# Kernel optimization log

Measured on AMD Instinct MI355X. Metric: run time of the kernel, lower is better.

## Reference

```python
import jax, jax.numpy as jnp
import numpy as np

W_DIM = 512
C_IN = 512
C_OUT = 512
K = 3
EPS = 1e-6
STYLE_SCALE = 1.0 / np.sqrt(W_DIM)              # EqualizedWeight scale for (out,in)
CONV_SCALE = 1.0 / np.sqrt(C_IN * K * K)        # EqualizedWeight scale for (out,in,k,k)


def setup_inputs() -> dict:
    key = jax.random.key(0)
    ks = jax.random.split(key, 6)
    B, H, W = 16, 64, 64
    return {
        "x": jax.random.normal(ks[0], (B, C_IN, H, W), dtype=jnp.float32),
        "w": jax.random.normal(ks[1], (B, W_DIM), dtype=jnp.float32),
        "style_weight": jax.random.normal(ks[2], (C_IN, W_DIM), dtype=jnp.float32),
        "style_bias": jnp.zeros((C_IN,), dtype=jnp.float32),
        "conv_weight": jax.random.normal(ks[3], (C_OUT, C_IN, K, K), dtype=jnp.float32),
        "noise_weight": jax.random.normal(ks[4], (1, C_OUT, 1, 1), dtype=jnp.float32),
        "bias": jnp.zeros((C_OUT,), dtype=jnp.float32),
        "noise": jax.random.normal(ks[5], (B, 1, H, W), dtype=jnp.float32),
    }


def reference(x, w, style_weight, style_bias, conv_weight, noise_weight, bias, noise):
    B, _, H, Wd = x.shape
    # to_style: equalized linear  [B, C_IN]
    s = w @ (style_weight * STYLE_SCALE).T + style_bias
    # modulate: [B, C_OUT, C_IN, K, K]
    wts = (conv_weight * CONV_SCALE)[None] * s[:, None, :, None, None]
    # demodulate
    sigma = jax.lax.rsqrt(jnp.sum(wts * wts, axis=(2, 3, 4)) + EPS)  # [B, C_OUT]
    wts = wts * sigma[:, :, None, None, None]
    # grouped conv with groups = batch
    x_r = x.reshape(1, B * C_IN, H, Wd)
    w_r = wts.reshape(B * C_OUT, C_IN, K, K)
    y = jax.lax.conv_general_dilated(
        x_r, w_r, window_strides=(1, 1), padding=[(1, 1), (1, 1)],
        dimension_numbers=("NCHW", "OIHW", "NCHW"), feature_group_count=B,
    ).reshape(B, C_OUT, H, Wd)
    # noise injection + bias + leaky relu(0.2)
    y = y + noise_weight * noise + bias[None, :, None, None]
    return jax.nn.leaky_relu(y, negative_slope=0.2)
```

## Files before the change

### kernel.cpp

```cpp
#include <hip/hip_runtime.h>


typedef __attribute__((ext_vector_type(8))) short short8;
typedef __attribute__((ext_vector_type(4))) float f32x4;

#define STYLE_SCALE 0.044194173824159216f
#define CONV_SCALE  0.014731391274719742f
#define CS2         (1.0f/4608.0f)

static __device__ __forceinline__ unsigned short f2bf(float x) {
    union { float f; unsigned int u; } a; a.f = x;
    unsigned int r = a.u + 0x7fffu + ((a.u >> 16) & 1u);
    return (unsigned short)(r >> 16);
}

static __device__ __forceinline__ void gl_lds16(const void* g, void* l) {
    __builtin_amdgcn_global_load_lds(
        (const __attribute__((address_space(1))) unsigned int*)g,
        (__attribute__((address_space(3))) unsigned int*)l, 16, 0, 0);
}

__global__ void k_style(const float* __restrict__ w, const float* __restrict__ sw,
                        const float* __restrict__ sb, float* __restrict__ s) {
    int b = blockIdx.x, t = threadIdx.x;
    __shared__ float wl[512];
    wl[t]       = w[b*512 + t];
    wl[t + 256] = w[b*512 + t + 256];
    __syncthreads();
    for (int j = t; j < 512; j += 256) {
        const float4* row = (const float4*)(sw + j*512);
        float acc = 0.f;
#pragma unroll 4
        for (int k = 0; k < 128; ++k) {
            float4 v = row[k];
            acc += v.x*wl[4*k] + v.y*wl[4*k+1] + v.z*wl[4*k+2] + v.w*wl[4*k+3];
        }
        s[b*512 + j] = acc * STYLE_SCALE + sb[j];
    }
}

__global__ void k_csq(const float* __restrict__ cw, float* __restrict__ csq) {
    int o = blockIdx.x, t = threadIdx.x;
    for (int i = t; i < 512; i += 256) {
        const float* p = cw + (size_t)(o*512 + i)*9;
        float a = 0.f;
#pragma unroll
        for (int k = 0; k < 9; ++k) { float v = p[k]; a += v*v; }
        csq[o*512 + i] = a * CS2;
    }
}

__global__ void k_sigma(const float* __restrict__ s, const float* __restrict__ csq,
                        float* __restrict__ sig) {
    int b = blockIdx.x, t = threadIdx.x;
    __shared__ float s2[512];
    float v0 = s[b*512 + t], v1 = s[b*512 + t + 256];
    s2[t] = v0*v0; s2[t+256] = v1*v1;
    __syncthreads();
    for (int o = t; o < 512; o += 256) {
        const float4* row = (const float4*)(csq + o*512);
        float acc = 0.f;
#pragma unroll 4
        for (int k = 0; k < 128; ++k) {
            float4 c = row[k];
            acc += c.x*s2[4*k] + c.y*s2[4*k+1] + c.z*s2[4*k+2] + c.w*s2[4*k+3];
        }
        sig[b*512 + o] = 1.0f / sqrtf(acc + 1e-6f);
    }
}

__global__ void k_xt(const float* __restrict__ x, const float* __restrict__ s,
                     unsigned short* __restrict__ xt) {
    int h = blockIdx.x, b = blockIdx.y, t = threadIdx.x;
    __shared__ float tile[64][65];
    for (int c0 = 0; c0 < 512; c0 += 64) {
        for (int it = 0; it < 16; ++it) {
            int idx = t + it*256, c = idx >> 6, wq = idx & 63;
            tile[c][wq] = x[((size_t)(b*512 + c0 + c)*64 + h)*64 + wq];
        }
        __syncthreads();
        for (int it = 0; it < 4; ++it) {
            int idx = t + it*256;
            int wq = idx >> 4, c = (idx & 15) * 4;
            float s0 = s[b*512 + c0 + c],     s1 = s[b*512 + c0 + c + 1];
            float s2v = s[b*512 + c0 + c + 2], s3 = s[b*512 + c0 + c + 3];
            ushort4 pk;
            pk.x = f2bf(tile[c][wq]   * s0);
            pk.y = f2bf(tile[c+1][wq] * s1);
            pk.z = f2bf(tile[c+2][wq] * s2v);
            pk.w = f2bf(tile[c+3][wq] * s3);
            *(ushort4*)(xt + ((size_t)(b*4096 + h*64 + wq)*512 + c0 + c)) = pk;
        }
        __syncthreads();
    }
}

__global__ void k_cwt(const float* __restrict__ cw, unsigned short* __restrict__ cwt) {
    int p = blockIdx.x;
    int g = p & 3, pt = p >> 2;
    int tap = pt % 9, ic = pt / 9;
    int i0 = ic*32 + g*8;
    int t = threadIdx.x;
    for (int o = t; o < 512; o += 256) {
        union { unsigned short us[8]; uint4 q; } u;
#pragma unroll
        for (int j = 0; j < 8; ++j)
            u.us[j] = f2bf(cw[((size_t)o*512 + i0 + j)*9 + tap] * CONV_SCALE);
        *(uint4*)(cwt + ((size_t)p*512 + o)*8) = u.q;
    }
}

__global__ __launch_bounds__(256, 2)
void k_conv(const unsigned short* __restrict__ xt, const unsigned short* __restrict__ cwt,
            const float* __restrict__ sig, const float* __restrict__ nw,
            const float* __restrict__ bias, const float* __restrict__ noise,
            float* __restrict__ out) {
    __shared__ short xs_s[6*66*32];
    __shared__ short wsm_s[9*4*64*8];

    const int tid  = threadIdx.x;
    const int lane = tid & 63;
    const int wave = tid >> 6;
    const int quad = lane >> 4;
    const int l15  = lane & 15;

    const int b     = blockIdx.y;
    const int oblk  = blockIdx.x & 7;
    const int pxblk = blockIdx.x >> 3;
    const int o0 = oblk * 64, h0 = pxblk * 4;

    for (int i = tid; i < 6*66*32/2; i += 256) ((unsigned int*)xs_s)[i] = 0u;
    __syncthreads();

    f32x4 acc[4][4];
#pragma unroll
    for (int mt = 0; mt < 4; ++mt)
#pragma unroll
        for (int nt = 0; nt < 4; ++nt) acc[mt][nt] = (f32x4){0.f, 0.f, 0.f, 0.f};

    for (int ic = 0; ic < 16; ++ic) {
        for (int q = wave; q < 60; q += 4) {
            if (q < 36) {
                const unsigned short* src = cwt + ((size_t)(ic*36 + q)*512 + o0 + lane)*8;
                gl_lds16(src, wsm_s + q*512);
            } else {
                int xq = q - 36;
                int r = xq >> 2, p0 = (xq & 3) << 4;
                int gr = h0 - 1 + r;
                if (gr >= 0 && gr < 64) {
                    int p  = p0 + (lane >> 2);
                    int cg = (lane & 3) ^ ((lane >> 2) & 3);
                    const unsigned short* src =
                        xt + ((size_t)(b*4096 + gr*64 + p)*512 + ic*32 + cg*8);
                    gl_lds16(src, xs_s + (r*66 + 1 + p0)*32);
                }
            }
        }
        __syncthreads();

#pragma unroll
        for (int tap = 0; tap < 9; ++tap) {
            const int dy = tap / 3, dx = tap % 3;
            short8 af[4], bfr[4];
            const short8* wp = (const short8*)wsm_s;
            const short8* xp = (const short8*)xs_s;
#pragma unroll
            for (int mt = 0; mt < 4; ++mt)
                af[mt] = wp[(tap*4 + quad)*64 + mt*16 + l15];
#pragma unroll
            for (int nt = 0; nt < 4; ++nt) {
                int wc   = nt*16 + l15 + dx - 1;
                int col  = wc + 1;
                int slot = quad ^ (wc & 3);
                bfr[nt] = xp[((wave + dy)*66 + col)*4 + slot];
            }
#pragma unroll
            for (int mt = 0; mt < 4; ++mt)
#pragma unroll
                for (int nt = 0; nt < 4; ++nt)
                    acc[mt][nt] = __builtin_amdgcn_mfma_f32_16x16x32_bf16(
                        af[mt], bfr[nt], acc[mt][nt], 0, 0, 0);
        }
        __syncthreads();
    }

    const int h = h0 + wave;
    float nz[4];
#pragma unroll
    for (int nt = 0; nt < 4; ++nt) nz[nt] = noise[b*4096 + h*64 + nt*16 + l15];
#pragma unroll
    for (int mt = 0; mt < 4; ++mt) {
#pragma unroll
        for (int r = 0; r < 4; ++r) {
            int o = o0 + mt*16 + quad*4 + r;
            float sg = sig[b*512 + o];
            float nwv = nw[o], bv = bias[o];
#pragma unroll
            for (int nt = 0; nt < 4; ++nt) {
                float v = acc[mt][nt][r] * sg + nwv * nz[nt] + bv;
                v = (v >= 0.f) ? v : 0.2f * v;
                out[((size_t)(b*512 + o)*4096) + h*64 + nt*16 + l15] = v;
            }
        }
    }
}

extern "C" void kernel_launch(void* const* d_in, const int* in_sizes, int n_in,
                              void* d_out, int out_size, void* d_ws, size_t ws_size,
                              hipStream_t stream) {
    const float* x     = (const float*)d_in[0];
    const float* w     = (const float*)d_in[1];
    const float* sw    = (const float*)d_in[2];
    const float* sb    = (const float*)d_in[3];
    const float* cw    = (const float*)d_in[4];
    const float* nw    = (const float*)d_in[5];
    const float* bias  = (const float*)d_in[6];
    const float* noise = (const float*)d_in[7];
    float* out = (float*)d_out;

    char* ws = (char*)d_ws;
    unsigned short* xt  = (unsigned short*)(ws + 0);
    unsigned short* cwt = (unsigned short*)(ws + 67108864);
    float* s   = (float*)(ws + 71827456);
    float* sig = (float*)(ws + 71860224);
    float* csq = (float*)(ws + 71892992);

    k_style<<<16, 256, 0, stream>>>(w, sw, sb, s);
    k_csq  <<<512, 256, 0, stream>>>(cw, csq);
    k_sigma<<<16, 256, 0, stream>>>(s, csq, sig);
    k_xt   <<<dim3(64, 16), 256, 0, stream>>>(x, s, xt);
    k_cwt  <<<576, 256, 0, stream>>>(cw, cwt);
    k_conv <<<dim3(128, 16), 256, 0, stream>>>(xt, cwt, sig, nw, bias, noise, out);
}
```

Measured before the change: 578.4 us.

## Double conv rows per block, fuse weight prep, parallelize style/sigma kernels

The conv kernel now computes 8 output rows per block with two accumulator sets, reusing each LDS weight tile across twice as many pixels and halving the grid. The csq and cwt weight preprocessing kernels are merged into one kernel that stages a weight row in LDS. The style and sigma matvecs are split across more blocks with a partial-sum reduction, and the x transpose uses vectorized loads and 8-wide bf16 stores. The cost is higher register pressure and LDS use per conv block, which may reduce occupancy.

```diff
diff --git a/kernel.cpp b/kernel.cpp
--- a/kernel.cpp
+++ b/kernel.cpp
@@ -22,91 +22,105 @@
 
 __global__ void k_style(const float* __restrict__ w, const float* __restrict__ sw,
                         const float* __restrict__ sb, float* __restrict__ s) {
-    int b = blockIdx.x, t = threadIdx.x;
+    int b = blockIdx.y, j0 = blockIdx.x * 64, t = threadIdx.x;
     __shared__ float wl[512];
-    wl[t]       = w[b*512 + t];
-    wl[t + 256] = w[b*512 + t + 256];
-    __syncthreads();
-    for (int j = t; j < 512; j += 256) {
-        const float4* row = (const float4*)(sw + j*512);
-        float acc = 0.f;
+    __shared__ float part[256];
+    wl[t] = w[b*512 + t]; wl[t+256] = w[b*512 + t + 256];
+    __syncthreads();
+    int jl = t & 63, seg = t >> 6;
+    const float4* row = (const float4*)(sw + (size_t)(j0 + jl)*512) + seg*32;
+    const float*  wv  = wl + seg*128;
+    float acc = 0.f;
 #pragma unroll 4
-        for (int k = 0; k < 128; ++k) {
-            float4 v = row[k];
-            acc += v.x*wl[4*k] + v.y*wl[4*k+1] + v.z*wl[4*k+2] + v.w*wl[4*k+3];
-        }
-        s[b*512 + j] = acc * STYLE_SCALE + sb[j];
-    }
-}
-
-__global__ void k_csq(const float* __restrict__ cw, float* __restrict__ csq) {
+    for (int k = 0; k < 32; ++k) {
+        float4 v = row[k];
+        acc += v.x*wv[4*k] + v.y*wv[4*k+1] + v.z*wv[4*k+2] + v.w*wv[4*k+3];
+    }
+    part[t] = acc;
+    __syncthreads();
+    if (t < 64)
+        s[b*512 + j0 + t] = (part[t] + part[t+64] + part[t+128] + part[t+192])
+                            * STYLE_SCALE + sb[j0 + t];
+}
+
+__global__ void k_wprep(const float* __restrict__ cw, float* __restrict__ csq,
+                        unsigned short* __restrict__ cwt) {
     int o = blockIdx.x, t = threadIdx.x;
-    for (int i = t; i < 512; i += 256) {
-        const float* p = cw + (size_t)(o*512 + i)*9;
+    __shared__ float row[4608];
+    const float4* src = (const float4*)(cw + (size_t)o*4608);
+    for (int i = t; i < 1152; i += 256) ((float4*)row)[i] = src[i];
+    __syncthreads();
+#pragma unroll
+    for (int it = 0; it < 2; ++it) {
+        int i = t + it*256;
         float a = 0.f;
 #pragma unroll
-        for (int k = 0; k < 9; ++k) { float v = p[k]; a += v*v; }
-        csq[o*512 + i] = a * CS2;
+        for (int k = 0; k < 9; ++k) { float v = row[i*9 + k]; a += v*v; }
+        csq[(size_t)o*512 + i] = a * CS2;
+    }
+    for (int p = t; p < 576; p += 256) {
+        int ic = p / 36, rem = p % 36;
+        int tap = rem >> 2, g = rem & 3;
+        int i0 = ic*32 + g*8;
+        union { unsigned short us[8]; uint4 q; } u;
+#pragma unroll
+        for (int j = 0; j < 8; ++j)
+            u.us[j] = f2bf(row[(i0 + j)*9 + tap] * CONV_SCALE);
+        *(uint4*)(cwt + ((size_t)p*512 + o)*8) = u.q;
     }
 }
 
 __global__ void k_sigma(const float* __restrict__ s, const float* __restrict__ csq,
                         float* __restrict__ sig) {
-    int b = blockIdx.x, t = threadIdx.x;
-    __shared__ float s2[512];
+    int b = blockIdx.y, o0 = blockIdx.x * 64, t = threadIdx.x;
+    __shared__ float s2l[512];
+    __shared__ float part[256];
     float v0 = s[b*512 + t], v1 = s[b*512 + t + 256];
-    s2[t] = v0*v0; s2[t+256] = v1*v1;
-    __syncthreads();
-    for (int o = t; o < 512; o += 256) {
-        const float4* row = (const float4*)(csq + o*512);
-        float acc = 0.f;
+    s2l[t] = v0*v0; s2l[t+256] = v1*v1;
+    __syncthreads();
+    int ol = t & 63, seg = t >> 6;
+    const float4* row = (const float4*)(csq + (size_t)(o0 + ol)*512) + seg*32;
+    const float*  sv  = s2l + seg*128;
+    float acc = 0.f;
 #pragma unroll 4
-        for (int k = 0; k < 128; ++k) {
-            float4 c = row[k];
-            acc += c.x*s2[4*k] + c.y*s2[4*k+1] + c.z*s2[4*k+2] + c.w*s2[4*k+3];
-        }
-        sig[b*512 + o] = 1.0f / sqrtf(acc + 1e-6f);
-    }
+    for (int k = 0; k < 32; ++k) {
+        float4 c = row[k];
+        acc += c.x*sv[4*k] + c.y*sv[4*k+1] + c.z*sv[4*k+2] + c.w*sv[4*k+3];
+    }
+    part[t] = acc;
+    __syncthreads();
+    if (t < 64)
+        sig[b*512 + o0 + t] = 1.0f / sqrtf(part[t] + part[t+64] + part[t+128]
+                                           + part[t+192] + 1e-6f);
 }
 
 __global__ void k_xt(const float* __restrict__ x, const float* __restrict__ s,
                      unsigned short* __restrict__ xt) {
     int h = blockIdx.x, b = blockIdx.y, t = threadIdx.x;
     __shared__ float tile[64][65];
+    __shared__ float sl[64];
     for (int c0 = 0; c0 < 512; c0 += 64) {
-        for (int it = 0; it < 16; ++it) {
-            int idx = t + it*256, c = idx >> 6, wq = idx & 63;
-            tile[c][wq] = x[((size_t)(b*512 + c0 + c)*64 + h)*64 + wq];
-        }
-        __syncthreads();
+        if (t < 64) sl[t] = s[b*512 + c0 + t];
+#pragma unroll
         for (int it = 0; it < 4; ++it) {
             int idx = t + it*256;
-            int wq = idx >> 4, c = (idx & 15) * 4;
-            float s0 = s[b*512 + c0 + c],     s1 = s[b*512 + c0 + c + 1];
-            float s2v = s[b*512 + c0 + c + 2], s3 = s[b*512 + c0 + c + 3];
-            ushort4 pk;
-            pk.x = f2bf(tile[c][wq]   * s0);
-            pk.y = f2bf(tile[c+1][wq] * s1);
-            pk.z = f2bf(tile[c+2][wq] * s2v);
-            pk.w = f2bf(tile[c+3][wq] * s3);
-            *(ushort4*)(xt + ((size_t)(b*4096 + h*64 + wq)*512 + c0 + c)) = pk;
-        }
-        __syncthreads();
-    }
-}
-
-__global__ void k_cwt(const float* __restrict__ cw, unsigned short* __restrict__ cwt) {
-    int p = blockIdx.x;
-    int g = p & 3, pt = p >> 2;
-    int tap = pt % 9, ic = pt / 9;
-    int i0 = ic*32 + g*8;
-    int t = threadIdx.x;
-    for (int o = t; o < 512; o += 256) {
-        union { unsigned short us[8]; uint4 q; } u;
-#pragma unroll
-        for (int j = 0; j < 8; ++j)
-            u.us[j] = f2bf(cw[((size_t)o*512 + i0 + j)*9 + tap] * CONV_SCALE);
-        *(uint4*)(cwt + ((size_t)p*512 + o)*8) = u.q;
+            int c = idx >> 4, w4 = (idx & 15) * 4;
+            float4 v = *(const float4*)(x + ((size_t)(b*512 + c0 + c)*4096) + h*64 + w4);
+            tile[c][w4]   = v.x; tile[c][w4+1] = v.y;
+            tile[c][w4+2] = v.z; tile[c][w4+3] = v.w;
+        }
+        __syncthreads();
+#pragma unroll
+        for (int it = 0; it < 2; ++it) {
+            int idx = t + it*256;
+            int wq = idx >> 3, c = (idx & 7) * 8;
+            union { unsigned short us[8]; uint4 q; } u;
+#pragma unroll
+            for (int j = 0; j < 8; ++j)
+                u.us[j] = f2bf(tile[c + j][wq] * sl[c + j]);
+            *(uint4*)(xt + ((size_t)(b*4096 + h*64 + wq)*512 + c0 + c)) = u.q;
+        }
+        __syncthreads();
     }
 }
 
@@ -115,7 +129,7 @@
             const float* __restrict__ sig, const float* __restrict__ nw,
             const float* __restrict__ bias, const float* __restrict__ noise,
             float* __restrict__ out) {
-    __shared__ short xs_s[6*66*32];
+    __shared__ short xs_s[10*66*32];
     __shared__ short wsm_s[9*4*64*8];
 
     const int tid  = threadIdx.x;
@@ -127,19 +141,21 @@
     const int b     = blockIdx.y;
     const int oblk  = blockIdx.x & 7;
     const int pxblk = blockIdx.x >> 3;
-    const int o0 = oblk * 64, h0 = pxblk * 4;
-
-    for (int i = tid; i < 6*66*32/2; i += 256) ((unsigned int*)xs_s)[i] = 0u;
-    __syncthreads();
-
-    f32x4 acc[4][4];
-#pragma unroll
-    for (int mt = 0; mt < 4; ++mt)
-#pragma unroll
-        for (int nt = 0; nt < 4; ++nt) acc[mt][nt] = (f32x4){0.f, 0.f, 0.f, 0.f};
+    const int o0 = oblk * 64, h0 = pxblk * 8;
+
+    for (int i = tid; i < 10*66*32/2; i += 256) ((unsigned int*)xs_s)[i] = 0u;
+    __syncthreads();
+
+    f32x4 acc[2][4][4];
+#pragma unroll
+    for (int rr = 0; rr < 2; ++rr)
+#pragma unroll
+        for (int mt = 0; mt < 4; ++mt)
+#pragma unroll
+            for (int nt = 0; nt < 4; ++nt) acc[rr][mt][nt] = (f32x4){0.f,0.f,0.f,0.f};
 
     for (int ic = 0; ic < 16; ++ic) {
-        for (int q = wave; q < 60; q += 4) {
+        for (int q = wave; q < 76; q += 4) {
             if (q < 36) {
                 const unsigned short* src = cwt + ((size_t)(ic*36 + q)*512 + o0 + lane)*8;
                 gl_lds16(src, wsm_s + q*512);
@@ -161,45 +177,57 @@
 #pragma unroll
         for (int tap = 0; tap < 9; ++tap) {
             const int dy = tap / 3, dx = tap % 3;
-            short8 af[4], bfr[4];
+            short8 af[4];
             const short8* wp = (const short8*)wsm_s;
             const short8* xp = (const short8*)xs_s;
 #pragma unroll
             for (int mt = 0; mt < 4; ++mt)
                 af[mt] = wp[(tap*4 + quad)*64 + mt*16 + l15];
 #pragma unroll
-            for (int nt = 0; nt < 4; ++nt) {
-                int wc   = nt*16 + l15 + dx - 1;
-                int col  = wc + 1;
-                int slot = quad ^ (wc & 3);
-                bfr[nt] = xp[((wave + dy)*66 + col)*4 + slot];
+            for (int rr = 0; rr < 2; ++rr) {
+                const int row = wave + rr*4 + dy;
+                short8 bfr[4];
+#pragma unroll
+                for (int nt = 0; nt < 4; ++nt) {
+                    int wc   = nt*16 + l15 + dx - 1;
+                    int col  = wc + 1;
+                    int slot = quad ^ (wc & 3);
+                    bfr[nt] = xp[(row*66 + col)*4 + slot];
+                }
+#pragma unroll
+                for (int mt = 0; mt < 4; ++mt)
+#pragma unroll
+                    for (int nt = 0; nt < 4; ++nt)
+                        acc[rr][mt][nt] = __builtin_amdgcn_mfma_f32_16x16x32_bf16(
+                            af[mt], bfr[nt], acc[rr][mt][nt], 0, 0, 0);
             }
-#pragma unroll
-            for (int mt = 0; mt < 4; ++mt)
-#pragma unroll
-                for (int nt = 0; nt < 4; ++nt)
-                    acc[mt][nt] = __builtin_amdgcn_mfma_f32_16x16x32_bf16(
-                        af[mt], bfr[nt], acc[mt][nt], 0, 0, 0);
-        }
-        __syncthreads();
-    }
-
-    const int h = h0 + wave;
-    float nz[4];
-#pragma unroll
-    for (int nt = 0; nt < 4; ++nt) nz[nt] = noise[b*4096 + h*64 + nt*16 + l15];
+        }
+        __syncthreads();
+    }
+
+    float nz[2][4];
+#pragma unroll
+    for (int rr = 0; rr < 2; ++rr) {
+        int h = h0 + wave + rr*4;
+#pragma unroll
+        for (int nt = 0; nt < 4; ++nt) nz[rr][nt] = noise[b*4096 + h*64 + nt*16 + l15];
+    }
 #pragma unroll
     for (int mt = 0; mt < 4; ++mt) {
 #pragma unroll
         for (int r = 0; r < 4; ++r) {
             int o = o0 + mt*16 + quad*4 + r;
-            float sg = sig[b*512 + o];
+            float sg  = sig[b*512 + o];
             float nwv = nw[o], bv = bias[o];
 #pragma unroll
-            for (int nt = 0; nt < 4; ++nt) {
-                float v = acc[mt][nt][r] * sg + nwv * nz[nt] + bv;
-                v = (v >= 0.f) ? v : 0.2f * v;
-                out[((size_t)(b*512 + o)*4096) + h*64 + nt*16 + l15] = v;
+            for (int rr = 0; rr < 2; ++rr) {
+                int h = h0 + wave + rr*4;
+#pragma unroll
+                for (int nt = 0; nt < 4; ++nt) {
+                    float v = acc[rr][mt][nt][r] * sg + nwv * nz[rr][nt] + bv;
+                    v = (v >= 0.f) ? v : 0.2f * v;
+                    out[((size_t)(b*512 + o)*4096) + h*64 + nt*16 + l15] = v;
+                }
             }
         }
     }
@@ -225,10 +253,9 @@
     float* sig = (float*)(ws + 71860224);
     float* csq = (float*)(ws + 71892992);
 
-    k_style<<<16, 256, 0, stream>>>(w, sw, sb, s);
-    k_csq  <<<512, 256, 0, stream>>>(cw, csq);
-    k_sigma<<<16, 256, 0, stream>>>(s, csq, sig);
+    k_wprep<<<512, 256, 0, stream>>>(cw, csq, cwt);
+    k_style<<<dim3(8, 16), 256, 0, stream>>>(w, sw, sb, s);
+    k_sigma<<<dim3(8, 16), 256, 0, stream>>>(s, csq, sig);
     k_xt   <<<dim3(64, 16), 256, 0, stream>>>(x, s, xt);
-    k_cwt  <<<576, 256, 0, stream>>>(cw, cwt);
-    k_conv <<<dim3(128, 16), 256, 0, stream>>>(xt, cwt, sig, nw, bias, noise, out);
-}
+    k_conv <<<dim3(64, 16), 256, 0, stream>>>(xt, cwt, sig, nw, bias, noise, out);
+}
```

Measured after the change: 491.8 us. 15.0% less time.
